# Optimization experiments

Measured on AMD Instinct MI355X. Metric: run time of the kernel, lower is better.

## Reference

```python
import jax, jax.numpy as jnp
import numpy as np

N, D, B, E, H = 512, 32, 4, 256, 4
SEP = 256
HD = E // H


def setup_inputs() -> dict:
    key = jax.random.key(0)
    ks = jax.random.split(key, 8)
    s = 0.02
    return {
        "src": jax.random.normal(ks[0], (N, D, B, E), dtype=jnp.float32),
        "w_in_row": jax.random.normal(ks[1], (3 * E, E), dtype=jnp.float32) * s,
        "b_in_row": jnp.zeros((3 * E,), jnp.float32),
        "w_out_row": jax.random.normal(ks[2], (E, E), dtype=jnp.float32) * s,
        "b_out_row": jnp.zeros((E,), jnp.float32),
        "w_in_col": jax.random.normal(ks[3], (3 * E, E), dtype=jnp.float32) * s,
        "b_in_col": jnp.zeros((3 * E,), jnp.float32),
        "w_out_col": jax.random.normal(ks[4], (E, E), dtype=jnp.float32) * s,
        "b_out_col": jnp.zeros((E,), jnp.float32),
        "ln_g": jnp.ones((E,), jnp.float32),
        "ln_b": jnp.zeros((E,), jnp.float32),
        "task_ids": jax.random.randint(ks[5], (B,), 0, 10),
        "single_eval_position": SEP,
    }


def _mha(x, w_in, b_in, w_out, b_out, mask):
    # x: (S, Bt, E); torch MultiheadAttention with batch_first=False
    S, Bt, _ = x.shape
    qkv = x @ w_in.T + b_in                      # (S, Bt, 3E)
    q, k, v = jnp.split(qkv, 3, axis=-1)
    to_heads = lambda t: t.reshape(S, Bt, H, HD).transpose(1, 2, 0, 3)  # (Bt,H,S,HD)
    q, k, v = to_heads(q), to_heads(k), to_heads(v)
    scores = jnp.einsum('bhqd,bhkd->bhqk', q, k) * (HD ** -0.5)
    if mask is not None:  # mask True == disallowed (torch convention)
        scores = jnp.where(mask[None, None], -jnp.inf, scores)
    attn = jax.nn.softmax(scores, axis=-1)
    out = jnp.einsum('bhqk,bhkd->bhqd', attn, v)
    out = out.transpose(2, 0, 1, 3).reshape(S, Bt, E)
    return out @ w_out.T + b_out


def _layer_norm(x, g, b, eps=1e-5):
    mu = x.mean(-1, keepdims=True)
    var = ((x - mu) ** 2).mean(-1, keepdims=True)
    return (x - mu) / jnp.sqrt(var + eps) * g + b


def reference(src, w_in_row, b_in_row, w_out_row, b_out_row,
              w_in_col, b_in_col, w_out_col, b_out_col,
              ln_g, ln_b, task_ids, single_eval_position):
    sep = single_eval_position
    idx = jnp.arange(N)
    # block mask: test queries may not attend to test keys
    row_mask = (idx[:, None] >= sep) & (idx[None, :] >= sep)
    # row attention over the N axis, batched across D*B
    src_row = _mha(src.reshape(N, D * B, E), w_in_row, b_in_row,
                   w_out_row, b_out_row, row_mask).reshape(N, D, B, E)
    # column attention over the D axis, batched across N*B (no mask)
    x_col = src.transpose(1, 0, 2, 3).reshape(D, N * B, E)
    src_col = _mha(x_col, w_in_col, b_in_col, w_out_col, b_out_col,
                   None).reshape(D, N, B, E).transpose(1, 0, 2, 3)
    # parallel axial (seq_axial=False), post-norm (pre_norm=False): row_norm unused
    return _layer_norm(src + src_row + src_col, ln_g, ln_b)
```

## Files before the change

### kernel.cpp

```cpp
#include <hip/hip_runtime.h>
#include <hip/hip_bf16.h>
#include <cstdint>
#include <cstddef>


typedef __hip_bfloat16 bf16;
typedef __attribute__((ext_vector_type(8))) short bf16x8;
typedef __attribute__((ext_vector_type(8))) short short8;
typedef __attribute__((ext_vector_type(4))) short bf16x4;
typedef __attribute__((ext_vector_type(4))) float f32x4;

#define NN 512
#define DD 32
#define BB 4
#define EE 256
#define HH 4
#define HDIM 64
#define DB (DD*BB)
#define MTOK (NN*DD*BB)
#define KBLK 64
#define QSCALE 0.1803368801f

extern "C" __device__ float __ocml_exp2_f32(float);

__device__ __forceinline__ float bf2f(bf16 x){ return __bfloat162float(x); }
__device__ __forceinline__ short pkbf(float x){
  union { float f; uint32_t u; } c; c.f = x;
  return (short)((c.u + 0x8000u) >> 16);
}

#define AS1C(p) ((const __attribute__((address_space(1))) void*)(p))
#define AS3(p)  ((__attribute__((address_space(3))) void*)(p))

__global__ __launch_bounds__(256) void cvt_main(
    const float* __restrict__ src, const float* __restrict__ wirf,
    const float* __restrict__ wicf, bf16* __restrict__ src_bf,
    bf16* __restrict__ wir, bf16* __restrict__ wic)
{
  const int b = blockIdx.x;
  const float* s; bf16* d; int off;
  if (b < 8192)      { s = src;  d = src_bf; off = b; }
  else if (b < 8288) { s = wirf; d = wir;    off = b - 8192; }
  else               { s = wicf; d = wic;    off = b - 8288; }
  const int i = (off * 256 + threadIdx.x) * 8;
  const float* p = s + i;
  short8 o;
  #pragma unroll
  for (int j = 0; j < 8; ++j) ((short*)&o)[j] = pkbf(p[j]);
  *(short8*)(d + i) = o;
}

__global__ __launch_bounds__(256) void cvt_w2_kernel(
    const float* __restrict__ orr, const float* __restrict__ oc,
    bf16* __restrict__ d_or, bf16* __restrict__ d_oc)
{
  const int b = blockIdx.x;
  const float* src = (b < 32) ? orr : oc;
  bf16* dst = (b < 32) ? d_or : d_oc;
  const int off = (b < 32) ? b : b - 32;
  const int i = (off * 256 + threadIdx.x) * 8;
  const float* p = src + i;
  short8 o;
  #pragma unroll
  for (int j = 0; j < 8; ++j) ((short*)&o)[j] = pkbf(p[j]);
  *(short8*)(dst + i) = o;
}

template<int NT>
__global__ __launch_bounds__(256,2) void gemm_qkv(
    const bf16* __restrict__ A, const bf16* __restrict__ W1,
    const bf16* __restrict__ W2, const float* __restrict__ b1,
    const float* __restrict__ b2, bf16* __restrict__ C,
    const int nt1, const int nout)
{
  __shared__ bf16 As[128][64];
  __shared__ bf16 Bs[128][64];
  const int bid = blockIdx.x;
  const int xcd = bid & 7;
  const int i0  = bid >> 3;
  const int bm  = xcd * 64 + i0 / NT;
  const int bn  = i0 % NT;
  const int lbn = (bn < nt1) ? bn : bn - nt1;
  const bf16* W = (bn < nt1) ? W1 : W2;
  const float* bias = (bn < nt1) ? b1 : b2;

  const int tid  = threadIdx.x;
  const int wid  = tid >> 6;
  const int lane = tid & 63;
  const int lo = lane & 15, hi = lane >> 4;
  const int wr = wid >> 1, wc = wid & 1;

  const int srow = lane >> 3;
  const int ssrc = ((lane & 7) << 4) ^ (srow << 4);

  f32x4 acc[4][4] = {};

  for (int k0 = 0; k0 < 256; k0 += 64) {
    __syncthreads();
    #pragma unroll
    for (int i = 0; i < 4; ++i) {
      const int r = wid * 32 + i * 8 + srow;
      const int m = bm * 128 + r;
      const char* gpA = (const char*)(A + (size_t)m * EE + k0) + ssrc;
      __builtin_amdgcn_global_load_lds(AS1C(gpA), AS3(&As[wid*32 + i*8][0]), 16, 0, 0);
      const int wn = lbn * 128 + r;
      const char* gpB = (const char*)(W + (size_t)wn * EE + k0) + ssrc;
      __builtin_amdgcn_global_load_lds(AS1C(gpB), AS3(&Bs[wid*32 + i*8][0]), 16, 0, 0);
    }
    __syncthreads();

    #pragma unroll
    for (int kc = 0; kc < 2; ++kc) {
      const int cc = kc * 64 + hi * 16;
      bf16x8 af[4], bfr[4];
      #pragma unroll
      for (int i = 0; i < 4; ++i) {
        const int ra = wr * 64 + i * 16 + lo;
        af[i]  = *(const bf16x8*)((const char*)&As[ra][0] + (cc ^ ((ra & 7) << 4)));
        const int rb = wc * 64 + i * 16 + lo;
        bfr[i] = *(const bf16x8*)((const char*)&Bs[rb][0] + (cc ^ ((rb & 7) << 4)));
      }
      __builtin_amdgcn_s_setprio(1);
      #pragma unroll
      for (int mi = 0; mi < 4; ++mi)
        #pragma unroll
        for (int ni = 0; ni < 4; ++ni)
          acc[mi][ni] = __builtin_amdgcn_mfma_f32_16x16x32_bf16(
              af[mi], bfr[ni], acc[mi][ni], 0, 0, 0);
      __builtin_amdgcn_s_setprio(0);
    }
  }

  float bv[4];
  #pragma unroll
  for (int ni = 0; ni < 4; ++ni)
    bv[ni] = bias[lbn * 128 + wc * 64 + ni * 16 + lo];

  #pragma unroll
  for (int mi = 0; mi < 4; ++mi) {
    #pragma unroll
    for (int r = 0; r < 4; ++r) {
      const int m = bm * 128 + wr * 64 + mi * 16 + hi * 4 + r;
      #pragma unroll
      for (int ni = 0; ni < 4; ++ni) {
        const int col = bn * 128 + wc * 64 + ni * 16 + lo;
        C[(size_t)m * nout + col] = __hip_bfloat16_raw{(unsigned short)pkbf(acc[mi][ni][r] + bv[ni])};
      }
    }
  }
}

__global__ __launch_bounds__(256,2) void gemm_oproj(
    const bf16* __restrict__ A1, const bf16* __restrict__ A2,
    const bf16* __restrict__ W1, const bf16* __restrict__ W2,
    const float* __restrict__ b1, const float* __restrict__ b2,
    bf16* __restrict__ C)
{
  __shared__ bf16 As[128][64];
  __shared__ bf16 Bs[128][64];
  const int bid = blockIdx.x;
  const int xcd = bid & 7;
  const int i0  = bid >> 3;
  const int bm  = xcd * 64 + (i0 >> 1);
  const int bn  = i0 & 1;

  const int tid  = threadIdx.x;
  const int wid  = tid >> 6;
  const int lane = tid & 63;
  const int lo = lane & 15, hi = lane >> 4;
  const int wr = wid >> 1, wc = wid & 1;

  const int srow = lane >> 3;
  const int ssrc = ((lane & 7) << 4) ^ (srow << 4);

  f32x4 acc[4][4] = {};

  for (int k0 = 0; k0 < 512; k0 += 64) {
    const bf16* A = (k0 < 256) ? A1 : A2;
    const bf16* W = (k0 < 256) ? W1 : W2;
    const int kk = k0 & 255;
    __syncthreads();
    #pragma unroll
    for (int i = 0; i < 4; ++i) {
      const int r = wid * 32 + i * 8 + srow;
      const int m = bm * 128 + r;
      const char* gpA = (const char*)(A + (size_t)m * EE + kk) + ssrc;
      __builtin_amdgcn_global_load_lds(AS1C(gpA), AS3(&As[wid*32 + i*8][0]), 16, 0, 0);
      const int wn = bn * 128 + r;
      const char* gpB = (const char*)(W + (size_t)wn * EE + kk) + ssrc;
      __builtin_amdgcn_global_load_lds(AS1C(gpB), AS3(&Bs[wid*32 + i*8][0]), 16, 0, 0);
    }
    __syncthreads();

    #pragma unroll
    for (int kc = 0; kc < 2; ++kc) {
      const int cc = kc * 64 + hi * 16;
      bf16x8 af[4], bfr[4];
      #pragma unroll
      for (int i = 0; i < 4; ++i) {
        const int ra = wr * 64 + i * 16 + lo;
        af[i]  = *(const bf16x8*)((const char*)&As[ra][0] + (cc ^ ((ra & 7) << 4)));
        const int rb = wc * 64 + i * 16 + lo;
        bfr[i] = *(const bf16x8*)((const char*)&Bs[rb][0] + (cc ^ ((rb & 7) << 4)));
      }
      __builtin_amdgcn_s_setprio(1);
      #pragma unroll
      for (int mi = 0; mi < 4; ++mi)
        #pragma unroll
        for (int ni = 0; ni < 4; ++ni)
          acc[mi][ni] = __builtin_amdgcn_mfma_f32_16x16x32_bf16(
              af[mi], bfr[ni], acc[mi][ni], 0, 0, 0);
      __builtin_amdgcn_s_setprio(0);
    }
  }

  float bv[4];
  #pragma unroll
  for (int ni = 0; ni < 4; ++ni) {
    const int col = bn * 128 + wc * 64 + ni * 16 + lo;
    bv[ni] = b1[col] + b2[col];
  }

  #pragma unroll
  for (int mi = 0; mi < 4; ++mi) {
    #pragma unroll
    for (int r = 0; r < 4; ++r) {
      const int m = bm * 128 + wr * 64 + mi * 16 + hi * 4 + r;
      #pragma unroll
      for (int ni = 0; ni < 4; ++ni) {
        const int col = bn * 128 + wc * 64 + ni * 16 + lo;
        C[(size_t)m * EE + col] = __hip_bfloat16_raw{(unsigned short)pkbf(acc[mi][ni][r] + bv[ni])};
      }
    }
  }
}

__global__ __launch_bounds__(256,3) void attn_axial(
    const bf16* __restrict__ baseR, const bf16* __restrict__ baseC,
    const int stride, bf16* __restrict__ attnR, bf16* __restrict__ attnC,
    const int* __restrict__ sep_ptr, const int nrow)
{
  __shared__ bf16 smem[9216];
  const int tid  = threadIdx.x;
  const int lane = tid & 63;
  const int lo = lane & 15, hi = lane >> 4;

  if ((int)blockIdx.x < nrow) {
    const int bid = blockIdx.x;
    const int xcd = bid & 7;
    const int idx = bid >> 3;
    const int pair = xcd * 64 + (idx >> 2);
    const int qt = idx & 3;
    const int t = pair >> 2;
    const int h = pair & 3;
    const int sep = *sep_ptr;
    const int wid = tid >> 6;
    bf16* Ks = smem;
    bf16* Vt = smem + 4608;

    const int qb = qt * 128;
    const int q0 = qb + wid * 32;

    bf16x8 qf[2][2];
    #pragma unroll
    for (int mf = 0; mf < 2; ++mf) {
      const bf16* Qp = baseR + ((size_t)(q0 + mf*16 + lo) * DB + t) * stride + h * HDIM;
      bf16x8 a = *(const bf16x8*)(Qp + hi * 8);
      bf16x8 b = *(const bf16x8*)(Qp + 32 + hi * 8);
      #pragma unroll
      for (int j = 0; j < 8; ++j) {
        ((short*)&qf[mf][0])[j] = pkbf(bf2f(((const bf16*)&a)[j]) * QSCALE);
        ((short*)&qf[mf][1])[j] = pkbf(bf2f(((const bf16*)&b)[j]) * QSCALE);
      }
    }

    const int kr  = tid >> 2;
    const int kc4 = (tid & 3) * 16;
    const int vr  = tid & 63;
    const int vc  = (tid >> 6) * 16;
    const bf16* Kbase = baseR + ((size_t)kr * DB + t) * stride + EE + h * HDIM + kc4;
    const bf16* Vbase = baseR + ((size_t)vr * DB + t) * stride + 2*EE + h * HDIM + vc;
    const size_t kstep = (size_t)KBLK * DB * stride;

    f32x4 Oa[2][4] = {};
    float l_run[2] = {0.f, 0.f};

    const int nkt = (qb >= sep) ? ((sep + KBLK - 1) >> 6) : (NN >> 6);
    const bool need_mask = (qb + 128 > sep) && (nkt * KBLK > sep);

    bf16x8 kg0 = *(const bf16x8*)(Kbase);
    bf16x8 kg1 = *(const bf16x8*)(Kbase + 8);
    bf16x8 vg0 = *(const bf16x8*)(Vbase);
    bf16x8 vg1 = *(const bf16x8*)(Vbase + 8);

    for (int kt = 0; kt < nkt; ++kt) {
      const int k0 = kt * KBLK;

      *(bf16x8*)&Ks[kr*72 + kc4]     = kg0;
      *(bf16x8*)&Ks[kr*72 + kc4 + 8] = kg1;
      #pragma unroll
      for (int j = 0; j < 8; ++j) {
        Vt[(vc + j)*72 + vr]     = ((const bf16*)&vg0)[j];
        Vt[(vc + 8 + j)*72 + vr] = ((const bf16*)&vg1)[j];
      }
      __syncthreads();

      if (kt + 1 < nkt) {
        const size_t off = (size_t)(kt + 1) * kstep;
        kg0 = *(const bf16x8*)(Kbase + off);
        kg1 = *(const bf16x8*)(Kbase + off + 8);
        vg0 = *(const bf16x8*)(Vbase + off);
        vg1 = *(const bf16x8*)(Vbase + off + 8);
      }

      f32x4 st[2][4];
      #pragma unroll
      for (int kb = 0; kb < 4; ++kb) {
        bf16x8 kf0 = *(const bf16x8*)&Ks[(kb*16 + lo)*72 + hi*8];
        bf16x8 kf1 = *(const bf16x8*)&Ks[(kb*16 + lo)*72 + 32 + hi*8];
        __builtin_amdgcn_s_setprio(1);
        st[0][kb] = __builtin_amdgcn_mfma_f32_16x16x32_bf16(kf0, qf[0][0], (f32x4){0,0,0,0}, 0, 0, 0);
        st[0][kb] = __builtin_amdgcn_mfma_f32_16x16x32_bf16(kf1, qf[0][1], st[0][kb], 0, 0, 0);
        st[1][kb] = __builtin_amdgcn_mfma_f32_16x16x32_bf16(kf0, qf[1][0], (f32x4){0,0,0,0}, 0, 0, 0);
        st[1][kb] = __builtin_amdgcn_mfma_f32_16x16x32_bf16(kf1, qf[1][1], st[1][kb], 0, 0, 0);
        __builtin_amdgcn_s_setprio(0);
      }

      if (need_mask && k0 + KBLK > sep) {
        #pragma unroll
        for (int mf = 0; mf < 2; ++mf) {
          const int qq = q0 + mf*16 + lo;
          #pragma unroll
          for (int kb = 0; kb < 4; ++kb)
            #pragma unroll
            for (int r = 0; r < 4; ++r) {
              const int kk = k0 + kb*16 + 4*hi + r;
              if (qq >= sep && kk >= sep) st[mf][kb][r] = -1e30f;
            }
        }
      }

      bf16x8 pa[2][2];
      #pragma unroll
      for (int mf = 0; mf < 2; ++mf) {
        float s0 = 0.f;
        #pragma unroll
        for (int kb = 0; kb < 4; ++kb)
          #pragma unroll
          for (int r = 0; r < 4; ++r) {
            const float pv = __ocml_exp2_f32(st[mf][kb][r]);
            st[mf][kb][r] = pv;
            s0 += pv;
          }
        l_run[mf] += s0;

        #pragma unroll
        for (int kc = 0; kc < 2; ++kc)
          #pragma unroll
          for (int j = 0; j < 8; ++j)
            ((short*)&pa[mf][kc])[j] = pkbf(st[mf][kc*2 + (j>>2)][j&3]);
      }

      __builtin_amdgcn_s_setprio(1);
      #pragma unroll
      for (int n = 0; n < 4; ++n) {
        #pragma unroll
        for (int kc = 0; kc < 2; ++kc) {
          const bf16* vrow = &Vt[(n*16 + lo)*72];
          bf16x4 v0 = *(const bf16x4*)(vrow + kc*32 + 4*hi);
          bf16x4 v1 = *(const bf16x4*)(vrow + kc*32 + 16 + 4*hi);
          bf16x8 vf = __builtin_shufflevector(v0, v1, 0,1,2,3,4,5,6,7);
          Oa[0][n] = __builtin_amdgcn_mfma_f32_16x16x32_bf16(pa[0][kc], vf, Oa[0][n], 0, 0, 0);
          Oa[1][n] = __builtin_amdgcn_mfma_f32_16x16x32_bf16(pa[1][kc], vf, Oa[1][n], 0, 0, 0);
        }
      }
      __builtin_amdgcn_s_setprio(0);
      __syncthreads();
    }

    #pragma unroll
    for (int mf = 0; mf < 2; ++mf) {
      float lt = l_run[mf];
      lt += __shfl_xor(lt, 16);
      lt += __shfl_xor(lt, 32);
      float linv[4];
      #pragma unroll
      for (int r = 0; r < 4; ++r) linv[r] = 1.f / __shfl(lt, hi*4 + r);
      #pragma unroll
      for (int r = 0; r < 4; ++r) {
        const int qq = q0 + mf*16 + hi*4 + r;
        bf16* Op = attnR + ((size_t)qq * DB + t) * EE + h * HDIM;
        #pragma unroll
        for (int n = 0; n < 4; ++n)
          Op[n*16 + lo] = __hip_bfloat16_raw{(unsigned short)pkbf(Oa[mf][n][r] * linv[r])};
      }
    }
  } else {
    const int cb = blockIdx.x - nrow;
    const int n = cb >> 2;
    const int b = cb & 3;
    const int h = tid >> 6;

    {
      const int k  = tid & 31;
      const int hh = tid >> 6;
      const int dh = ((tid >> 5) & 1) * 32;
      const bf16* Vp = baseC + ((size_t)(n*DB + k*4 + b)) * stride + 2*EE + hh*64 + dh;
      #pragma unroll
      for (int c = 0; c < 4; ++c) {
        bf16x8 vv = *(const bf16x8*)(Vp + c*8);
        #pragma unroll
        for (int j = 0; j < 8; ++j)
          smem[hh*2304 + (dh + c*8 + j)*36 + k] = ((const bf16*)&vv)[j];
      }
    }

    bf16x8 qf[2][2], kf[2][2];
    #pragma unroll
    for (int mt = 0; mt < 2; ++mt) {
      const bf16* Qp = baseC + ((size_t)(n*DB + (mt*16 + lo)*4 + b)) * stride + h*64;
      #pragma unroll
      for (int kc = 0; kc < 2; ++kc) {
        bf16x8 v = *(const bf16x8*)(Qp + kc*32 + hi*8);
        #pragma unroll
        for (int j = 0; j < 8; ++j)
          ((short*)&v)[j] = pkbf(bf2f(((const bf16*)&v)[j]) * QSCALE);
        qf[mt][kc] = v;
      }
      const bf16* Kp = Qp + EE;
      kf[mt][0] = *(const bf16x8*)(Kp + hi*8);
      kf[mt][1] = *(const bf16x8*)(Kp + 32 + hi*8);
    }
    __syncthreads();

    f32x4 st[2][2];
    #pragma unroll
    for (int kt = 0; kt < 2; ++kt)
      #pragma unroll
      for (int mt = 0; mt < 2; ++mt) {
        f32x4 a = {0,0,0,0};
        a = __builtin_amdgcn_mfma_f32_16x16x32_bf16(kf[kt][0], qf[mt][0], a, 0, 0, 0);
        a = __builtin_amdgcn_mfma_f32_16x16x32_bf16(kf[kt][1], qf[mt][1], a, 0, 0, 0);
        st[kt][mt] = a;
      }

    float l[2];
    #pragma unroll
    for (int mt = 0; mt < 2; ++mt) {
      float s0 = 0.f;
      #pragma unroll
      for (int kt = 0; kt < 2; ++kt)
        #pragma unroll
        for (int r = 0; r < 4; ++r) {
          const float pv = __ocml_exp2_f32(st[kt][mt][r]);
          st[kt][mt][r] = pv;
          s0 += pv;
        }
      s0 += __shfl_xor(s0, 16);
      s0 += __shfl_xor(s0, 32);
      l[mt] = s0;
    }

    bf16x8 pa[2];
    #pragma unroll
    for (int mt = 0; mt < 2; ++mt)
      #pragma unroll
      for (int j = 0; j < 8; ++j)
        ((short*)&pa[mt])[j] = pkbf(st[j>>2][mt][j&3]);

    f32x4 Oa[2][4] = {};
    #pragma unroll
    for (int nn = 0; nn < 4; ++nn) {
      const bf16* vrow = &smem[h*2304 + (nn*16 + lo)*36];
      bf16x4 v0 = *(const bf16x4*)(vrow + 4*hi);
      bf16x4 v1 = *(const bf16x4*)(vrow + 16 + 4*hi);
      bf16x8 vf = __builtin_shufflevector(v0, v1, 0,1,2,3,4,5,6,7);
      Oa[0][nn] = __builtin_amdgcn_mfma_f32_16x16x32_bf16(pa[0], vf, Oa[0][nn], 0, 0, 0);
      Oa[1][nn] = __builtin_amdgcn_mfma_f32_16x16x32_bf16(pa[1], vf, Oa[1][nn], 0, 0, 0);
    }

    float linv[2][4];
    #pragma unroll
    for (int mt = 0; mt < 2; ++mt)
      #pragma unroll
      for (int r = 0; r < 4; ++r)
        linv[mt][r] = 1.f / __shfl(l[mt], hi*4 + r);
    #pragma unroll
    for (int mt = 0; mt < 2; ++mt) {
      #pragma unroll
      for (int r = 0; r < 4; ++r) {
        const int q = mt*16 + hi*4 + r;
        bf16* Op = attnC + ((size_t)(n*DB + q*4 + b)) * EE + h*64;
        #pragma unroll
        for (int nn = 0; nn < 4; ++nn)
          Op[nn*16 + lo] = __hip_bfloat16_raw{(unsigned short)pkbf(Oa[mt][nn][r] * linv[mt][r])};
      }
    }
  }
}

__global__ __launch_bounds__(256) void ln_kernel(
    const float* __restrict__ src, const bf16* __restrict__ rc,
    const float* __restrict__ g, const float* __restrict__ b,
    float* __restrict__ out)
{
  const int m = blockIdx.x * 4 + (threadIdx.x >> 6);
  const int lane = threadIdx.x & 63;
  const float4 s4 = ((const float4*)src)[(size_t)m*64 + lane];
  const bf16x4 r4 = ((const bf16x4*)rc)[(size_t)m*64 + lane];
  float x[4];
  x[0] = s4.x + bf2f(((const bf16*)&r4)[0]);
  x[1] = s4.y + bf2f(((const bf16*)&r4)[1]);
  x[2] = s4.z + bf2f(((const bf16*)&r4)[2]);
  x[3] = s4.w + bf2f(((const bf16*)&r4)[3]);
  float sum = x[0] + x[1] + x[2] + x[3];
  #pragma unroll
  for (int off = 1; off < 64; off <<= 1) sum += __shfl_xor(sum, off);
  const float mu = sum * (1.f/EE);
  float d[4];
  #pragma unroll
  for (int j = 0; j < 4; ++j) d[j] = x[j] - mu;
  float ss = d[0]*d[0] + d[1]*d[1] + d[2]*d[2] + d[3]*d[3];
  #pragma unroll
  for (int off = 1; off < 64; off <<= 1) ss += __shfl_xor(ss, off);
  const float rstd = rsqrtf(ss * (1.f/EE) + 1e-5f);
  const float4 g4 = ((const float4*)g)[lane];
  const float4 b4 = ((const float4*)b)[lane];
  float4 o;
  o.x = d[0] * rstd * g4.x + b4.x;
  o.y = d[1] * rstd * g4.y + b4.y;
  o.z = d[2] * rstd * g4.z + b4.z;
  o.w = d[3] * rstd * g4.w + b4.w;
  ((float4*)out)[(size_t)m*64 + lane] = o;
}

extern "C" void kernel_launch(void* const* d_in, const int* in_sizes, int n_in,
                              void* d_out, int out_size, void* d_ws, size_t ws_size,
                              hipStream_t stream)
{
  const float* src      = (const float*)d_in[0];
  const float* w_in_row = (const float*)d_in[1];
  const float* b_in_row = (const float*)d_in[2];
  const float* w_out_row= (const float*)d_in[3];
  const float* b_out_row= (const float*)d_in[4];
  const float* w_in_col = (const float*)d_in[5];
  const float* b_in_col = (const float*)d_in[6];
  const float* w_out_col= (const float*)d_in[7];
  const float* b_out_col= (const float*)d_in[8];
  const float* ln_g     = (const float*)d_in[9];
  const float* ln_b     = (const float*)d_in[10];
  const int*   sep_ptr  = (const int*)d_in[12];
  float* out = (float*)d_out;

  char* ws = (char*)d_ws;
  dim3 blk(256);

  if (ws_size >= 268435456ULL) {
    bf16* qkv    = (bf16*)(ws);
    bf16* attnR  = (bf16*)(ws + 201326592);
    bf16* attnC  = (bf16*)(ws + 234881024);
    bf16* src_bf = attnR;
    bf16* wir    = (bf16*)(ws + 234881024);
    bf16* wic    = (bf16*)(ws + 235274240);
    bf16* wor    = (bf16*)(ws + 67108864);
    bf16* woc    = (bf16*)(ws + 67239936);
    bf16* rc     = (bf16*)(ws);

    cvt_main<<<dim3(8384), blk, 0, stream>>>(src, w_in_row, w_in_col,
                                             src_bf, wir, wic);
    gemm_qkv<12><<<dim3(512*12), blk, 0, stream>>>(
        src_bf, wir, wic, b_in_row, b_in_col, qkv, 6, 1536);
    attn_axial<<<dim3(4096), blk, 0, stream>>>(
        qkv, qkv + 768, 1536, attnR, attnC, sep_ptr, 2048);
    cvt_w2_kernel<<<dim3(64), blk, 0, stream>>>(w_out_row, w_out_col, wor, woc);
    gemm_oproj<<<dim3(1024), blk, 0, stream>>>(
        attnR, attnC, wor, woc, b_out_row, b_out_col, rc);
    ln_kernel<<<dim3(MTOK/4), blk, 0, stream>>>(src, rc, ln_g, ln_b, out);
  } else {
    bf16* qkv    = (bf16*)(ws);
    bf16* attnR  = (bf16*)(ws + 100663296);
    bf16* attnC  = (bf16*)(ws + 134217728);
    bf16* src_bf = (bf16*)(ws + 167772160);
    bf16* wir    = (bf16*)(ws + 201326592);
    bf16* wic    = (bf16*)(ws + 201719808);
    bf16* wor    = (bf16*)(ws + 67108864);
    bf16* woc    = (bf16*)(ws + 67239936);
    bf16* rc     = (bf16*)(ws);

    cvt_main<<<dim3(8384), blk, 0, stream>>>(src, w_in_row, w_in_col,
                                             src_bf, wir, wic);
    gemm_qkv<6><<<dim3(512*6), blk, 0, stream>>>(
        src_bf, wir, wir, b_in_row, b_in_row, qkv, 6, 768);
    attn_axial<<<dim3(2048), blk, 0, stream>>>(
        qkv, qkv, 768, attnR, attnC, sep_ptr, 2048);
    gemm_qkv<6><<<dim3(512*6), blk, 0, stream>>>(
        src_bf, wic, wic, b_in_col, b_in_col, qkv, 6, 768);
    attn_axial<<<dim3(2048), blk, 0, stream>>>(
        qkv, qkv, 768, attnR, attnC, sep_ptr, 0);
    cvt_w2_kernel<<<dim3(64), blk, 0, stream>>>(w_out_row, w_out_col, wor, woc);
    gemm_oproj<<<dim3(1024), blk, 0, stream>>>(
        attnR, attnC, wor, woc, b_out_row, b_out_col, rc);
    ln_kernel<<<dim3(MTOK/4), blk, 0, stream>>>(src, rc, ln_g, ln_b, out);
  }
}
```

Baseline: 238.3 us.

## Fuse fp32-to-bf16 src conversion into QKV GEMM A-tile loads

Drops the separate pass that converts the whole fp32 src tensor to bf16. The QKV GEMM now reads fp32 A rows into registers, converts them to bf16 and writes them into swizzled LDS, prefetching the next K slice while the MFMAs run. This removes a full write and re-read of the bf16 src copy (about 32 MB each way) and one launch. In exchange the GEMM reads twice the bytes for A, once per N-tile block (12 or 6 times), and carries more registers, which may hurt occupancy.

```diff
diff --git a/kernel.cpp b/kernel.cpp
--- a/kernel.cpp
+++ b/kernel.cpp
@@ -32,22 +32,20 @@
 #define AS1C(p) ((const __attribute__((address_space(1))) void*)(p))
 #define AS3(p)  ((__attribute__((address_space(3))) void*)(p))
 
-__global__ __launch_bounds__(256) void cvt_main(
-    const float* __restrict__ src, const float* __restrict__ wirf,
-    const float* __restrict__ wicf, bf16* __restrict__ src_bf,
-    bf16* __restrict__ wir, bf16* __restrict__ wic)
+__global__ __launch_bounds__(256) void cvt_w_kernel(
+    const float* __restrict__ ir, const float* __restrict__ ic,
+    bf16* __restrict__ d_ir, bf16* __restrict__ d_ic)
 {
   const int b = blockIdx.x;
-  const float* s; bf16* d; int off;
-  if (b < 8192)      { s = src;  d = src_bf; off = b; }
-  else if (b < 8288) { s = wirf; d = wir;    off = b - 8192; }
-  else               { s = wicf; d = wic;    off = b - 8288; }
+  const float* src = (b < 96) ? ir : ic;
+  bf16* dst = (b < 96) ? d_ir : d_ic;
+  const int off = (b < 96) ? b : b - 96;
   const int i = (off * 256 + threadIdx.x) * 8;
-  const float* p = s + i;
+  const float* p = src + i;
   short8 o;
   #pragma unroll
   for (int j = 0; j < 8; ++j) ((short*)&o)[j] = pkbf(p[j]);
-  *(short8*)(d + i) = o;
+  *(short8*)(dst + i) = o;
 }
 
 __global__ __launch_bounds__(256) void cvt_w2_kernel(
@@ -68,7 +66,7 @@
 
 template<int NT>
 __global__ __launch_bounds__(256,2) void gemm_qkv(
-    const bf16* __restrict__ A, const bf16* __restrict__ W1,
+    const float* __restrict__ A, const bf16* __restrict__ W1,
     const bf16* __restrict__ W2, const float* __restrict__ b1,
     const float* __restrict__ b2, bf16* __restrict__ C,
     const int nt1, const int nout)
@@ -91,7 +89,17 @@
   const int wr = wid >> 1, wc = wid & 1;
 
   const int srow = lane >> 3;
-  const int ssrc = ((lane & 7) << 4) ^ (srow << 4);
+  const int slin = (lane & 7) << 4;
+  const int ssrc = slin ^ (srow << 4);
+
+  float4 ar[4][2];
+  #pragma unroll
+  for (int i = 0; i < 4; ++i) {
+    const int m = bm * 128 + wid * 32 + i * 8 + srow;
+    const float* ap = A + (size_t)m * EE + (lane & 7) * 8;
+    ar[i][0] = ((const float4*)ap)[0];
+    ar[i][1] = ((const float4*)ap)[1];
+  }
 
   f32x4 acc[4][4] = {};
 
@@ -100,14 +108,28 @@
     #pragma unroll
     for (int i = 0; i < 4; ++i) {
       const int r = wid * 32 + i * 8 + srow;
-      const int m = bm * 128 + r;
-      const char* gpA = (const char*)(A + (size_t)m * EE + k0) + ssrc;
-      __builtin_amdgcn_global_load_lds(AS1C(gpA), AS3(&As[wid*32 + i*8][0]), 16, 0, 0);
       const int wn = lbn * 128 + r;
       const char* gpB = (const char*)(W + (size_t)wn * EE + k0) + ssrc;
       __builtin_amdgcn_global_load_lds(AS1C(gpB), AS3(&Bs[wid*32 + i*8][0]), 16, 0, 0);
+      bf16x8 av;
+      #pragma unroll
+      for (int j = 0; j < 4; ++j) {
+        ((short*)&av)[j]     = pkbf(((const float*)&ar[i][0])[j]);
+        ((short*)&av)[4 + j] = pkbf(((const float*)&ar[i][1])[j]);
+      }
+      *(bf16x8*)((char*)&As[r][0] + (slin ^ ((r & 7) << 4))) = av;
     }
     __syncthreads();
+
+    if (k0 + 64 < 256) {
+      #pragma unroll
+      for (int i = 0; i < 4; ++i) {
+        const int m = bm * 128 + wid * 32 + i * 8 + srow;
+        const float* ap = A + (size_t)m * EE + k0 + 64 + (lane & 7) * 8;
+        ar[i][0] = ((const float4*)ap)[0];
+        ar[i][1] = ((const float4*)ap)[1];
+      }
+    }
 
     #pragma unroll
     for (int kc = 0; kc < 2; ++kc) {
@@ -559,17 +581,15 @@
     bf16* qkv    = (bf16*)(ws);
     bf16* attnR  = (bf16*)(ws + 201326592);
     bf16* attnC  = (bf16*)(ws + 234881024);
-    bf16* src_bf = attnR;
-    bf16* wir    = (bf16*)(ws + 234881024);
-    bf16* wic    = (bf16*)(ws + 235274240);
+    bf16* wir    = (bf16*)(ws + 201326592);
+    bf16* wic    = (bf16*)(ws + 201719808);
     bf16* wor    = (bf16*)(ws + 67108864);
     bf16* woc    = (bf16*)(ws + 67239936);
     bf16* rc     = (bf16*)(ws);
 
-    cvt_main<<<dim3(8384), blk, 0, stream>>>(src, w_in_row, w_in_col,
-                                             src_bf, wir, wic);
+    cvt_w_kernel<<<dim3(192), blk, 0, stream>>>(w_in_row, w_in_col, wir, wic);
     gemm_qkv<12><<<dim3(512*12), blk, 0, stream>>>(
-        src_bf, wir, wic, b_in_row, b_in_col, qkv, 6, 1536);
+        src, wir, wic, b_in_row, b_in_col, qkv, 6, 1536);
     attn_axial<<<dim3(4096), blk, 0, stream>>>(
         qkv, qkv + 768, 1536, attnR, attnC, sep_ptr, 2048);
     cvt_w2_kernel<<<dim3(64), blk, 0, stream>>>(w_out_row, w_out_col, wor, woc);
@@ -580,21 +600,19 @@
     bf16* qkv    = (bf16*)(ws);
     bf16* attnR  = (bf16*)(ws + 100663296);
     bf16* attnC  = (bf16*)(ws + 134217728);
-    bf16* src_bf = (bf16*)(ws + 167772160);
-    bf16* wir    = (bf16*)(ws + 201326592);
-    bf16* wic    = (bf16*)(ws + 201719808);
+    bf16* wir    = (bf16*)(ws + 167772160);
+    bf16* wic    = (bf16*)(ws + 168165376);
     bf16* wor    = (bf16*)(ws + 67108864);
     bf16* woc    = (bf16*)(ws + 67239936);
     bf16* rc     = (bf16*)(ws);
 
-    cvt_main<<<dim3(8384), blk, 0, stream>>>(src, w_in_row, w_in_col,
-                                             src_bf, wir, wic);
+    cvt_w_kernel<<<dim3(192), blk, 0, stream>>>(w_in_row, w_in_col, wir, wic);
     gemm_qkv<6><<<dim3(512*6), blk, 0, stream>>>(
-        src_bf, wir, wir, b_in_row, b_in_row, qkv, 6, 768);
+        src, wir, wir, b_in_row, b_in_row, qkv, 6, 768);
     attn_axial<<<dim3(2048), blk, 0, stream>>>(
         qkv, qkv, 768, attnR, attnC, sep_ptr, 2048);
     gemm_qkv<6><<<dim3(512*6), blk, 0, stream>>>(
-        src_bf, wic, wic, b_in_col, b_in_col, qkv, 6, 768);
+        src, wic, wic, b_in_col, b_in_col, qkv, 6, 768);
     attn_axial<<<dim3(2048), blk, 0, stream>>>(
         qkv, qkv, 768, attnR, attnC, sep_ptr, 0);
     cvt_w2_kernel<<<dim3(64), blk, 0, stream>>>(w_out_row, w_out_col, wor, woc);
```

Result: slower. 264.1 us (+10.8%).
